# Kernel tuning notes

Hardware: AMD Instinct MI355X
Metric: run time of the kernel (lower is better)

Reference implementation:

```python
import jax, jax.numpy as jnp
import numpy as np

PHASE_1_START = 0
PHASE_2_START = 101
PHASE_3_START = 201


def _pair_sqdist_plus1(pairs):
    # pairs: [N, 2, D] -> d_i = ||p0 - p1||^2 + 1, shape [N]
    diff = pairs[:, 0, :] - pairs[:, 1, :]
    return jnp.sum(diff * diff, axis=-1) + 1.0


def _phase_weights(iteration):
    # iteration is a static Python int, so plain control flow is fine
    if iteration < PHASE_2_START:
        t1, t2 = float(PHASE_1_START), float(PHASE_2_START)
        frac = (t1 - 1.0) / (t2 - 1.0)
        return 2.0, 1000.0 * (1.0 - frac) + 3.0 * frac, 1.0
    elif iteration < PHASE_3_START:
        return 3.0, 3.0, 1.0
    else:
        return 1.0, 0.0, 1.0


def setup_inputs() -> dict:
    key = jax.random.key(0)
    k1, k2, k3 = jax.random.split(key, 3)
    return {
        "neighbor_pairs": jax.random.normal(k1, (5_000_000, 2, 2), dtype=jnp.float32),
        "midnear_pairs": jax.random.normal(k2, (2_500_000, 2, 2), dtype=jnp.float32),
        "far_pairs": jax.random.normal(k3, (10_000_000, 2, 2), dtype=jnp.float32),
        "iteration": 50,
    }


def reference(neighbor_pairs, midnear_pairs, far_pairs, iteration):
    w_n, w_m, w_f = _phase_weights(iteration)
    d_n = _pair_sqdist_plus1(neighbor_pairs)
    d_m = _pair_sqdist_plus1(midnear_pairs)
    d_f = _pair_sqdist_plus1(far_pairs)
    near_loss = jnp.sum(d_n / (10.0 + d_n)) * w_n
    midnear_loss = jnp.sum(d_m / (10000.0 + d_m)) * w_m
    far_loss = jnp.sum(1.0 / (1.0 + d_f)) * w_f
    return near_loss + midnear_loss + far_loss
```

## Files before the change

kernel.cpp:

```cpp
#include <hip/hip_runtime.h>

#define GRID 2048
#define BLK  256
#define NWAVES (BLK / 64)
#define STRIDE (GRID * BLK)

typedef float floatx4 __attribute__((ext_vector_type(4)));

__device__ __forceinline__ float frcp(float x) {
    return __builtin_amdgcn_rcpf(x);
}

__global__ __launch_bounds__(BLK) void pacmap_partial_kernel(
    const floatx4* __restrict__ nb, int n_n,
    const floatx4* __restrict__ mn, int n_m,
    const floatx4* __restrict__ fr, int n_f,
    float* __restrict__ ws) {

    const int tid = blockIdx.x * BLK + threadIdx.x;

    float s_n = 0.0f, s_m = 0.0f, s_f = 0.0f;

    auto do_near = [&]() {
        for (int i = tid; i < n_n; i += STRIDE) {
            floatx4 p = nb[i];
            float dx = p.x - p.z, dy = p.y - p.w;
            float d  = fmaf(dx, dx, fmaf(dy, dy, 1.0f));
            s_n += d * frcp(10.0f + d);
        }
    };
    auto do_mid = [&]() {
        for (int i = tid; i < n_m; i += STRIDE) {
            floatx4 p = mn[i];
            float dx = p.x - p.z, dy = p.y - p.w;
            float d  = fmaf(dx, dx, fmaf(dy, dy, 1.0f));
            s_m += d * frcp(10000.0f + d);
        }
    };
    auto do_far = [&]() {
        for (int i = tid; i < n_f; i += STRIDE) {
            floatx4 p = __builtin_nontemporal_load(&fr[i]);
            float dx = p.x - p.z, dy = p.y - p.w;
            float d  = fmaf(dx, dx, fmaf(dy, dy, 1.0f));
            s_f += frcp(1.0f + d);
        }
    };

    if (blockIdx.x & 1) {
        do_far();
        do_near();
        do_mid();
    } else {
        do_near();
        do_mid();
        do_far();
    }

    #pragma unroll
    for (int off = 32; off > 0; off >>= 1) {
        s_n += __shfl_down(s_n, off, 64);
        s_m += __shfl_down(s_m, off, 64);
        s_f += __shfl_down(s_f, off, 64);
    }

    __shared__ float sm[3][NWAVES];
    const int lane = threadIdx.x & 63;
    const int wid  = threadIdx.x >> 6;
    if (lane == 0) {
        sm[0][wid] = s_n;
        sm[1][wid] = s_m;
        sm[2][wid] = s_f;
    }
    __syncthreads();
    if (threadIdx.x == 0) {
        float a = 0.0f, b = 0.0f, c = 0.0f;
        #pragma unroll
        for (int i = 0; i < NWAVES; ++i) {
            a += sm[0][i];
            b += sm[1][i];
            c += sm[2][i];
        }
        ws[blockIdx.x]            = a;
        ws[GRID + blockIdx.x]     = b;
        ws[2 * GRID + blockIdx.x] = c;
    }
}

__global__ __launch_bounds__(BLK) void pacmap_finalize_kernel(
    const float* __restrict__ ws,
    const int* __restrict__ iter_p,
    float* __restrict__ out) {

    float s_n = 0.0f, s_m = 0.0f, s_f = 0.0f;
    for (int i = threadIdx.x; i < GRID; i += BLK) {
        s_n += ws[i];
        s_m += ws[GRID + i];
        s_f += ws[2 * GRID + i];
    }

    #pragma unroll
    for (int off = 32; off > 0; off >>= 1) {
        s_n += __shfl_down(s_n, off, 64);
        s_m += __shfl_down(s_m, off, 64);
        s_f += __shfl_down(s_f, off, 64);
    }

    __shared__ float sm[3][NWAVES];
    const int lane = threadIdx.x & 63;
    const int wid  = threadIdx.x >> 6;
    if (lane == 0) {
        sm[0][wid] = s_n;
        sm[1][wid] = s_m;
        sm[2][wid] = s_f;
    }
    __syncthreads();
    if (threadIdx.x == 0) {
        float a = 0.0f, b = 0.0f, c = 0.0f;
        #pragma unroll
        for (int i = 0; i < NWAVES; ++i) {
            a += sm[0][i];
            b += sm[1][i];
            c += sm[2][i];
        }

        const int it = *iter_p;
        float w_n, w_m, w_f;
        if (it < 101) {
            const float frac = (0.0f - 1.0f) / (101.0f - 1.0f);
            w_n = 2.0f;
            w_m = 1000.0f * (1.0f - frac) + 3.0f * frac;
            w_f = 1.0f;
        } else if (it < 201) {
            w_n = 3.0f; w_m = 3.0f; w_f = 1.0f;
        } else {
            w_n = 1.0f; w_m = 0.0f; w_f = 1.0f;
        }
        out[0] = a * w_n + b * w_m + c * w_f;
    }
}

extern "C" void kernel_launch(void* const* d_in, const int* in_sizes, int n_in,
                              void* d_out, int out_size, void* d_ws, size_t ws_size,
                              hipStream_t stream) {
    const floatx4* nb = (const floatx4*)d_in[0];
    const floatx4* mn = (const floatx4*)d_in[1];
    const floatx4* fr = (const floatx4*)d_in[2];
    const int* iter_p = (const int*)d_in[3];

    const int n_n = in_sizes[0] / 4;
    const int n_m = in_sizes[1] / 4;
    const int n_f = in_sizes[2] / 4;

    float* ws  = (float*)d_ws;
    float* out = (float*)d_out;

    pacmap_partial_kernel<<<GRID, BLK, 0, stream>>>(nb, n_n, mn, n_m, fr, n_f, ws);
    pacmap_finalize_kernel<<<1, BLK, 0, stream>>>(ws, iter_p, out);
}
```

Before: 285.6 us.

## Interleave all three pair streams in one fused loop with clamped loads

Replaces the three sequential grid-stride loops with a single loop that, per iteration, issues 4 far, 2 near and 1 mid 16-byte loads, sized in proportion to each array's length. Indices are clamped so every load is valid and out-of-range terms are masked to zero, with separate accumulators per slot. The aim is more independent memory requests in flight per thread to better saturate HBM bandwidth. In exchange it adds redundant clamped loads in tail iterations and more registers per thread.

```diff
diff --git a/kernel.cpp b/kernel.cpp
--- a/kernel.cpp
+++ b/kernel.cpp
@@ -11,6 +11,11 @@
     return __builtin_amdgcn_rcpf(x);
 }
 
+__device__ __forceinline__ float sqd1(floatx4 p) {
+    float dx = p.x - p.z, dy = p.y - p.w;
+    return fmaf(dx, dx, fmaf(dy, dy, 1.0f));
+}
+
 __global__ __launch_bounds__(BLK) void pacmap_partial_kernel(
     const floatx4* __restrict__ nb, int n_n,
     const floatx4* __restrict__ mn, int n_m,
@@ -19,42 +24,69 @@
 
     const int tid = blockIdx.x * BLK + threadIdx.x;
 
-    float s_n = 0.0f, s_m = 0.0f, s_f = 0.0f;
+    float s_n0 = 0.0f, s_n1 = 0.0f;
+    float s_m0 = 0.0f;
+    float s_f0 = 0.0f, s_f1 = 0.0f, s_f2 = 0.0f, s_f3 = 0.0f;
 
-    auto do_near = [&]() {
-        for (int i = tid; i < n_n; i += STRIDE) {
-            floatx4 p = nb[i];
-            float dx = p.x - p.z, dy = p.y - p.w;
-            float d  = fmaf(dx, dx, fmaf(dy, dy, 1.0f));
-            s_n += d * frcp(10.0f + d);
-        }
-    };
-    auto do_mid = [&]() {
-        for (int i = tid; i < n_m; i += STRIDE) {
-            floatx4 p = mn[i];
-            float dx = p.x - p.z, dy = p.y - p.w;
-            float d  = fmaf(dx, dx, fmaf(dy, dy, 1.0f));
-            s_m += d * frcp(10000.0f + d);
-        }
-    };
-    auto do_far = [&]() {
-        for (int i = tid; i < n_f; i += STRIDE) {
-            floatx4 p = __builtin_nontemporal_load(&fr[i]);
-            float dx = p.x - p.z, dy = p.y - p.w;
-            float d  = fmaf(dx, dx, fmaf(dy, dy, 1.0f));
-            s_f += frcp(1.0f + d);
-        }
-    };
+    const int rem_n = n_n - tid;
+    const int rem_m = n_m - tid;
+    const int rem_f = n_f - tid;
+    int it_n = rem_n > 0 ? (rem_n + 2 * STRIDE - 1) / (2 * STRIDE) : 0;
+    int it_m = rem_m > 0 ? (rem_m + STRIDE - 1) / STRIDE : 0;
+    int it_f = rem_f > 0 ? (rem_f + 4 * STRIDE - 1) / (4 * STRIDE) : 0;
+    int iters = max(it_n, max(it_m, it_f));
 
-    if (blockIdx.x & 1) {
-        do_far();
-        do_near();
-        do_mid();
-    } else {
-        do_near();
-        do_mid();
-        do_far();
+    int i_n = tid, i_m = tid, i_f = tid;
+
+    for (int k = 0; k < iters; ++k) {
+        const int in0 = i_n;
+        const int in1 = i_n + STRIDE;
+        const int im0 = i_m;
+        const int if0 = i_f;
+        const int if1 = i_f + STRIDE;
+        const int if2 = i_f + 2 * STRIDE;
+        const int if3 = i_f + 3 * STRIDE;
+
+        const int jn0 = min(in0, n_n - 1);
+        const int jn1 = min(in1, n_n - 1);
+        const int jm0 = min(im0, n_m - 1);
+        const int jf0 = min(if0, n_f - 1);
+        const int jf1 = min(if1, n_f - 1);
+        const int jf2 = min(if2, n_f - 1);
+        const int jf3 = min(if3, n_f - 1);
+
+        floatx4 pf0 = __builtin_nontemporal_load(&fr[jf0]);
+        floatx4 pf1 = __builtin_nontemporal_load(&fr[jf1]);
+        floatx4 pf2 = __builtin_nontemporal_load(&fr[jf2]);
+        floatx4 pf3 = __builtin_nontemporal_load(&fr[jf3]);
+        floatx4 pn0 = nb[jn0];
+        floatx4 pn1 = nb[jn1];
+        floatx4 pm0 = mn[jm0];
+
+        float dn0 = sqd1(pn0);
+        float dn1 = sqd1(pn1);
+        float dm0 = sqd1(pm0);
+        float df0 = sqd1(pf0);
+        float df1 = sqd1(pf1);
+        float df2 = sqd1(pf2);
+        float df3 = sqd1(pf3);
+
+        s_n0 += (in0 < n_n) ? dn0 * frcp(10.0f + dn0) : 0.0f;
+        s_n1 += (in1 < n_n) ? dn1 * frcp(10.0f + dn1) : 0.0f;
+        s_m0 += (im0 < n_m) ? dm0 * frcp(10000.0f + dm0) : 0.0f;
+        s_f0 += (if0 < n_f) ? frcp(1.0f + df0) : 0.0f;
+        s_f1 += (if1 < n_f) ? frcp(1.0f + df1) : 0.0f;
+        s_f2 += (if2 < n_f) ? frcp(1.0f + df2) : 0.0f;
+        s_f3 += (if3 < n_f) ? frcp(1.0f + df3) : 0.0f;
+
+        i_n += 2 * STRIDE;
+        i_m += STRIDE;
+        i_f += 4 * STRIDE;
     }
+
+    float s_n = s_n0 + s_n1;
+    float s_m = s_m0;
+    float s_f = (s_f0 + s_f1) + (s_f2 + s_f3);
 
     #pragma unroll
     for (int off = 32; off > 0; off >>= 1) {
```

Measured after the change: 292.6 us. +2.5%, slower.
